# Optimization experiments

Measured on AMD Instinct MI355X. Metric: run time of the kernel, lower is better.

Reference implementation:

```python
import jax, jax.numpy as jnp
import numpy as np

B, N, E, K, H = 4, 2048, 512, 16, 8
EMB = 2 * E  # MultiheadAttention embed_dim = input_enc * 2


def setup_inputs() -> dict:
    key = jax.random.key(0)
    ks = jax.random.split(key, 6)
    s = 0.02
    return {
        "x": jax.random.normal(ks[0], (B, N, E), jnp.float32),
        "x_enc": jax.random.normal(ks[1], (B, N, EMB), jnp.float32),
        "w_in": jax.random.normal(ks[2], (3 * EMB, EMB), jnp.float32) * s,
        "b_in": jnp.zeros((3 * EMB,), jnp.float32),
        "w_out": jax.random.normal(ks[3], (EMB, EMB), jnp.float32) * s,
        "b_out": jnp.zeros((EMB,), jnp.float32),
        "k": K,
    }


def _knn_mean(x, k):
    # x: (B, N, E). torch code transposes to (B, E, N) and treats the E channel
    # rows as the 'points' for kNN (distance matrix is (B, E, E)).
    xt = jnp.swapaxes(x, 1, 2)                      # (B, E, N)
    sq = jnp.sum(xt * xt, axis=-1)                  # (B, E)
    dist = sq[:, :, None] + sq[:, None, :] - 2.0 * jnp.einsum("ben,bfn->bef", xt, xt)
    idx = jax.lax.top_k(-dist, k)[1]                # (B, E, k) smallest distances
    # fused gather + mean: avoid the (B, E, E, N) expand from the torch code
    nbrs = jnp.take_along_axis(xt[:, None, :, :], idx[:, :, :, None], axis=2)  # (B, E, k, N)
    return jnp.swapaxes(jnp.mean(nbrs, axis=2), 1, 2)  # (B, N, E)


def _mha(q, kv, w_in, b_in, w_out, b_out, h):
    # faithful torch nn.MultiheadAttention (batch_first) forward
    wq, wk, wv = jnp.split(w_in, 3, axis=0)
    bq, bk, bv = jnp.split(b_in, 3, axis=0)
    Q = q @ wq.T + bq
    Kt = kv @ wk.T + bk
    V = kv @ wv.T + bv
    b, l, emb = Q.shape
    m = Kt.shape[1]
    d = emb // h

    def split_heads(t):
        return t.reshape(t.shape[0], t.shape[1], h, d).transpose(0, 2, 1, 3)

    Qh, Kh, Vh = split_heads(Q), split_heads(Kt), split_heads(V)
    scores = jnp.einsum("bhld,bhmd->bhlm", Qh, Kh) / jnp.sqrt(jnp.float32(d))
    att = jax.nn.softmax(scores, axis=-1)
    o = jnp.einsum("bhlm,bhmd->bhld", att, Vh)      # (B, H, L, d)
    o = o.transpose(0, 2, 1, 3).reshape(b, l, emb)
    return o @ w_out.T + b_out


def reference(x, x_enc, w_in, b_in, w_out, b_out, k):
    b, n, e = x.shape
    x_knn = _knn_mean(x, k)                          # (B, N, E)
    cat = jnp.concatenate([jnp.swapaxes(x, 1, 2), jnp.swapaxes(x_knn, 1, 2)], axis=-1)  # (B, E, 2N)
    # faithful to torch .view(-1, 2*E, N): row-interleaving reshape, NOT a transpose
    q = jnp.swapaxes(cat.reshape(b, 2 * e, n), 1, 2)  # (B, N, 2E)
    attn = _mha(q, x_enc, w_in, b_in, w_out, b_out, H)  # (B, N, 2E)
    return jnp.concatenate([q, attn], axis=1)         # (B, 2N, 2E)
```

## Files before the change

### kernel.cpp

```cpp
#include <hip/hip_runtime.h>
#include <hip/hip_bf16.h>

#define B_ 4
#define N_ 2048
#define E_ 512
#define EMB_ 1024
#define H_ 8
#define D_ 128
#define KNN_ 16

typedef short short8_t __attribute__((ext_vector_type(8)));
typedef short short4_t __attribute__((ext_vector_type(4)));
typedef float float2_t __attribute__((ext_vector_type(2)));
typedef float float4_t __attribute__((ext_vector_type(4)));
typedef float float16_t __attribute__((ext_vector_type(16)));
typedef unsigned int uint2_t __attribute__((ext_vector_type(2)));
typedef unsigned int uint4_t __attribute__((ext_vector_type(4)));

__device__ __forceinline__ short f2bf(float f) {
  unsigned u = __float_as_uint(f);
  unsigned r = u + 0x7fffu + ((u >> 16) & 1u);
  return (short)(r >> 16);
}

__device__ __forceinline__ unsigned pk2bf(float a, float b) {
  float2 f; f.x = a; f.y = b;
  __hip_bfloat162 h = __float22bfloat162_rn(f);
  return *(unsigned*)&h;
}

__device__ __forceinline__ float fexp2(float x) {
  return __builtin_amdgcn_exp2f(x);
}

__device__ __forceinline__ void gload16(const short* g, short* l) {
  __builtin_amdgcn_global_load_lds(
      (const __attribute__((address_space(1))) void*)g,
      (__attribute__((address_space(3))) void*)l, 16, 0, 0);
}

__device__ __forceinline__ float tree16(const float* __restrict__ bs) {
  float t1[8], t2[4];
#pragma unroll
  for (int l = 0; l < 8; l++) t1[l] = __fadd_rn(bs[2 * l], bs[2 * l + 1]);
#pragma unroll
  for (int l = 0; l < 4; l++) t2[l] = __fadd_rn(t1[2 * l], t1[2 * l + 1]);
  return __fadd_rn(__fadd_rn(t2[0], t2[1]), __fadd_rn(t2[2], t2[3]));
}

__global__ __launch_bounds__(64) void k_gram_sqnp(const float* __restrict__ x,
                                                  float* __restrict__ g,
                                                  float* __restrict__ part) {
  const int bx = blockIdx.x;
  const int b = blockIdx.y;
  if (bx >= 272) {
    const int idx = (bx - 272) * 64 + threadIdx.x;
    const int e = idx & (E_ - 1), blk = idx >> 9;
    const float* p = x + (size_t)b * N_ * E_ + (size_t)blk * 128 * E_ + e;
    float lane[16];
#pragma unroll
    for (int l = 0; l < 16; l++) {
      float pr[8];
#pragma unroll
      for (int j = 0; j < 8; j++) {
        float v = p[(size_t)(j * 16 + l) * E_];
        pr[j] = __fmul_rn(v, v);
      }
      float s01 = __fadd_rn(pr[0], pr[1]);
      float s23 = __fadd_rn(pr[2], pr[3]);
      float s45 = __fadd_rn(pr[4], pr[5]);
      float s67 = __fadd_rn(pr[6], pr[7]);
      lane[l] = __fadd_rn(__fadd_rn(s01, s23), __fadd_rn(s45, s67));
    }
    float bb[8];
#pragma unroll
    for (int l = 0; l < 8; l++) bb[l] = __fadd_rn(lane[l], lane[l + 8]);
    float cc[4];
#pragma unroll
    for (int l = 0; l < 4; l++) cc[l] = __fadd_rn(bb[l], bb[l + 4]);
    part[((size_t)b * E_ + e) * 16 + blk] =
        __fadd_rn(__fadd_rn(cc[0], cc[1]), __fadd_rn(cc[2], cc[3]));
    return;
  }
  __shared__ __align__(16) float Xs[2][32][68];
  int p = bx >> 1;
  const int jh = bx & 1;
  int ti = 0;
  while (p >= 16 - ti) { p -= 16 - ti; ti++; }
  const int tj = ti + p;
  const int i0 = ti * 32, j0 = tj * 32 + jh * 16;
  const int lane = threadIdx.x;
  const int li = lane & 7, lj = lane >> 3;
  const int cq = lane & 7, rn = lane >> 3;
  const int qj = lane & 3, rj = lane >> 2;
  const float* xb = x + (size_t)b * N_ * E_;

  float acc[4][2];
#pragma unroll
  for (int u = 0; u < 4; u++) { acc[u][0] = 0.f; acc[u][1] = 0.f; }

  float4_t gi[4], gj[2];
#pragma unroll
  for (int ps = 0; ps < 4; ps++) {
    const int n = ps * 8 + rn;
    gi[ps] = *(const float4_t*)(xb + (size_t)n * E_ + i0 + cq * 4);
  }
#pragma unroll
  for (int s = 0; s < 2; s++) {
    const int n = s * 16 + rj;
    gj[s] = *(const float4_t*)(xb + (size_t)n * E_ + j0 + qj * 4);
  }
#pragma unroll
  for (int ps = 0; ps < 4; ps++) {
    const int nn = ps * 8 + rn;
    *(float4_t*)&Xs[0][nn][(cq * 4) ^ ((nn & 7) << 2)] = gi[ps];
  }
#pragma unroll
  for (int s = 0; s < 2; s++) {
    const int nn = s * 16 + rj;
    *(float4_t*)&Xs[0][nn][32 + ((qj * 4) ^ ((nn & 3) << 2))] = gj[s];
  }

  for (int c = 0; c < 64; c++) {
    const int buf = c & 1;
    if (c < 63) {
      const int nb = (c + 1) * 32;
#pragma unroll
      for (int ps = 0; ps < 4; ps++) {
        const int n = nb + ps * 8 + rn;
        gi[ps] = *(const float4_t*)(xb + (size_t)n * E_ + i0 + cq * 4);
      }
#pragma unroll
      for (int s = 0; s < 2; s++) {
        const int n = nb + s * 16 + rj;
        gj[s] = *(const float4_t*)(xb + (size_t)n * E_ + j0 + qj * 4);
      }
    }
#pragma unroll
    for (int nn = 0; nn < 32; nn++) {
      const float4_t va = *(const float4_t*)
          &Xs[buf][nn][(li * 4) ^ ((nn & 7) << 2)];
      const float2_t vb = *(const float2_t*)
          &Xs[buf][nn][32 + (((lj >> 1) * 4) ^ ((nn & 3) << 2)) + (lj & 1) * 2];
#pragma unroll
      for (int u = 0; u < 4; u++) {
        acc[u][0] = __fadd_rn(acc[u][0], __fmul_rn(va[u], vb[0]));
        acc[u][1] = __fadd_rn(acc[u][1], __fmul_rn(va[u], vb[1]));
      }
    }
    if (c < 63) {
#pragma unroll
      for (int ps = 0; ps < 4; ps++) {
        const int nn = ps * 8 + rn;
        *(float4_t*)&Xs[buf ^ 1][nn][(cq * 4) ^ ((nn & 7) << 2)] = gi[ps];
      }
#pragma unroll
      for (int s = 0; s < 2; s++) {
        const int nn = s * 16 + rj;
        *(float4_t*)&Xs[buf ^ 1][nn][32 + ((qj * 4) ^ ((nn & 3) << 2))] = gj[s];
      }
    }
  }
  float* gb = g + (size_t)b * E_ * E_;
#pragma unroll
  for (int u = 0; u < 4; u++) {
#pragma unroll
    for (int v = 0; v < 2; v++) {
      const int i = i0 + li * 4 + u, j = j0 + lj * 2 + v;
      gb[(size_t)i * E_ + j] = acc[u][v];
      if (ti != tj) gb[(size_t)j * E_ + i] = acc[u][v];
    }
  }
}

__global__ __launch_bounds__(64) void k_topk(const float* __restrict__ part,
                                             const float* __restrict__ g,
                                             int* __restrict__ idxout) {
  const int bi = blockIdx.x;
  const int b = bi >> 9, i = bi & (E_ - 1);
  const int lane = threadIdx.x;
  const float* gb = g + ((size_t)b * E_ + i) * E_;
  const float* pb = part + ((size_t)b << 9) * 16;
  const float sqi = tree16(pb + (size_t)i * 16);
  const int base = lane * 8;
  float v[8];
#pragma unroll
  for (int u = 0; u < 8; u++) {
    const float sqj = tree16(pb + (size_t)(base + u) * 16);
    v[u] = __fsub_rn(__fadd_rn(sqi, sqj), __fmul_rn(2.0f, gb[base + u]));
  }
  for (int t = 0; t < KNN_; t++) {
    float best = 3.0e38f; int bidx = E_;
#pragma unroll
    for (int u = 0; u < 8; u++) {
      if (v[u] < best) { best = v[u]; bidx = base + u; }
    }
#pragma unroll
    for (int off = 1; off < 64; off <<= 1) {
      float ov = __shfl_xor(best, off);
      int oi = __shfl_xor(bidx, off);
      if (ov < best || (ov == best && oi < bidx)) { best = ov; bidx = oi; }
    }
    if (lane == 0) idxout[(size_t)bi * KNN_ + t] = bidx;
#pragma unroll
    for (int u = 0; u < 8; u++) {
      if (bidx == base + u) v[u] = 3.0e38f;
    }
  }
}

__global__ __launch_bounds__(256) void k_knnmean(const float* __restrict__ x,
                                                 const int* __restrict__ idx,
                                                 float* __restrict__ out,
                                                 short* __restrict__ Xq) {
  const int n = blockIdx.x, b = blockIdx.y;
  const int tid = threadIdx.x;
  __shared__ float xrow[E_];
  const float* xr = x + ((size_t)b * N_ + n) * E_;
  for (int i = tid; i < E_; i += 256) xrow[i] = xr[i];
  __syncthreads();
  float* orow = out + ((size_t)b * (2 * N_) + n) * EMB_;
  unsigned* qrow = (unsigned*)(Xq + ((size_t)b * N_ + n) * EMB_);
  for (int i = tid; i < E_; i += 256) {
    const int* id = idx + ((size_t)b * E_ + i) * KNN_;
    float s = 0.f;
#pragma unroll
    for (int t = 0; t < KNN_; t++) s = __fadd_rn(s, xrow[id[t]]);
    float2 w; w.x = xrow[i]; w.y = s * (1.0f / 16.0f);
    *(float2*)&orow[2 * i] = w;
    qrow[i] = pk2bf(w.x, w.y);
  }
}

__global__ __launch_bounds__(256) void k_cvt3(const float* __restrict__ xe,
                                              const float* __restrict__ wi,
                                              const float* __restrict__ wo,
                                              short* __restrict__ Xe,
                                              short* __restrict__ Wi,
                                              short* __restrict__ Wo) {
  const size_t t = (size_t)blockIdx.x * 256 + threadIdx.x;
  const float* src; short* dst;
  if (t < 1048576u) { src = xe + t * 8; dst = Xe + t * 8; }
  else if (t < 1048576u + 393216u) {
    const size_t r = t - 1048576u; src = wi + r * 8; dst = Wi + r * 8;
  } else {
    const size_t r = t - 1441792u; src = wo + r * 8; dst = Wo + r * 8;
  }
  float4 a = *(const float4*)src, b = *(const float4*)(src + 4);
  short8_t v;
  v[0] = f2bf(a.x); v[1] = f2bf(a.y); v[2] = f2bf(a.z); v[3] = f2bf(a.w);
  v[4] = f2bf(b.x); v[5] = f2bf(b.y); v[6] = f2bf(b.z); v[7] = f2bf(b.w);
  *(short8_t*)dst = v;
}

__global__ __launch_bounds__(256) void k_gemm_qkv(
    const short* __restrict__ Xq, const short* __restrict__ Xe,
    const short* __restrict__ Win, const float* __restrict__ b_in,
    short* __restrict__ Qb, short* __restrict__ Kb, short* __restrict__ Vb) {
  __shared__ __align__(16) short As[128 * 64];
  __shared__ __align__(16) short Bs[128 * 64];
  const int tid = threadIdx.x;
  const int z = blockIdx.z;
  const short* X = (z == 0) ? Xq : Xe;
  const short* W = Win + (size_t)z * EMB_ * EMB_;
  const float* bias = b_in + z * EMB_;
  const int row0 = blockIdx.x * 128, col0 = blockIdx.y * 128;
  const int l = tid & 63, lg = l >> 4, lq = l & 15;
  const int w = tid >> 6, wm = w >> 1, wn = w & 1;
  float4_t acc[4][4];
#pragma unroll
  for (int i = 0; i < 4; i++)
#pragma unroll
    for (int j = 0; j < 4; j++) {
      acc[i][j][0] = 0.f; acc[i][j][1] = 0.f; acc[i][j][2] = 0.f; acc[i][j][3] = 0.f;
    }

  int soff[4], ldsb[4];
#pragma unroll
  for (int ii = 0; ii < 4; ii++) {
    const int cid = ii * 256 + tid;
    const int r = cid >> 3, c = cid & 7;
    soff[ii] = r * EMB_ + ((c * 8) ^ ((r & 7) << 3));
    ldsb[ii] = (ii * 256 + w * 64) * 8;
  }
  const short* Xb = X + (size_t)row0 * EMB_;
  const short* Wb = W + (size_t)col0 * EMB_;

  for (int kt = 0; kt < 16; kt++) {
    __syncthreads();
#pragma unroll
    for (int ii = 0; ii < 4; ii++) {
      gload16(Xb + soff[ii] + kt * 64, As + ldsb[ii]);
      gload16(Wb + soff[ii] + kt * 64, Bs + ldsb[ii]);
    }
    __syncthreads();
#pragma unroll
    for (int kk = 0; kk < 2; kk++) {
      short8_t af[4], bf[4];
#pragma unroll
      for (int mi = 0; mi < 4; mi++) {
        const int r = wm * 64 + mi * 16 + lq;
        af[mi] = *(const short8_t*)&As[r * 64 + ((kk * 32 + lg * 8) ^ ((r & 7) << 3))];
      }
#pragma unroll
      for (int ni = 0; ni < 4; ni++) {
        const int r = wn * 64 + ni * 16 + lq;
        bf[ni] = *(const short8_t*)&Bs[r * 64 + ((kk * 32 + lg * 8) ^ ((r & 7) << 3))];
      }
#pragma unroll
      for (int mi = 0; mi < 4; mi++)
#pragma unroll
        for (int ni = 0; ni < 4; ni++)
          acc[mi][ni] = __builtin_amdgcn_mfma_f32_16x16x32_bf16(af[mi], bf[ni], acc[mi][ni], 0, 0, 0);
    }
  }
  short* Yb = (z == 0) ? Qb : ((z == 1) ? Kb : Vb);
#pragma unroll
  for (int ni = 0; ni < 4; ni++) {
    const int col = col0 + wn * 64 + ni * 16 + lq;
    const float bv = bias[col];
#pragma unroll
    for (int mi = 0; mi < 4; mi++) {
#pragma unroll
      for (int j = 0; j < 4; j++) {
        const int m = row0 + wm * 64 + mi * 16 + lg * 4 + j;
        const float v = acc[mi][ni][j] + bv;
        if (z < 2) {
          Yb[(size_t)m * EMB_ + col] = f2bf(v);
        } else {
          const int b2 = m >> 11, n2 = m & (N_ - 1);
          Yb[((size_t)b2 * EMB_ + col) * N_ + n2] = f2bf(v);
        }
      }
    }
  }
}

__global__ __launch_bounds__(256) void k_gemm_out(
    const short* __restrict__ X, const short* __restrict__ W,
    const float* __restrict__ bias, float* __restrict__ Yf) {
  __shared__ __align__(16) short As[128 * 64];
  __shared__ __align__(16) short Bs[128 * 64];
  const int tid = threadIdx.x;
  const int row0 = blockIdx.x * 128, col0 = blockIdx.y * 128;
  const int l = tid & 63, lg = l >> 4, lq = l & 15;
  const int w = tid >> 6, wm = w >> 1, wn = w & 1;
  float4_t acc[4][4];
#pragma unroll
  for (int i = 0; i < 4; i++)
#pragma unroll
    for (int j = 0; j < 4; j++) {
      acc[i][j][0] = 0.f; acc[i][j][1] = 0.f; acc[i][j][2] = 0.f; acc[i][j][3] = 0.f;
    }

  int soff[4], ldsb[4];
#pragma unroll
  for (int ii = 0; ii < 4; ii++) {
    const int cid = ii * 256 + tid;
    const int r = cid >> 3, c = cid & 7;
    soff[ii] = r * EMB_ + ((c * 8) ^ ((r & 7) << 3));
    ldsb[ii] = (ii * 256 + w * 64) * 8;
  }
  const short* Xb = X + (size_t)row0 * EMB_;
  const short* Wb = W + (size_t)col0 * EMB_;

  for (int kt = 0; kt < 16; kt++) {
    __syncthreads();
#pragma unroll
    for (int ii = 0; ii < 4; ii++) {
      gload16(Xb + soff[ii] + kt * 64, As + ldsb[ii]);
      gload16(Wb + soff[ii] + kt * 64, Bs + ldsb[ii]);
    }
    __syncthreads();
#pragma unroll
    for (int kk = 0; kk < 2; kk++) {
      short8_t af[4], bf[4];
#pragma unroll
      for (int mi = 0; mi < 4; mi++) {
        const int r = wm * 64 + mi * 16 + lq;
        af[mi] = *(const short8_t*)&As[r * 64 + ((kk * 32 + lg * 8) ^ ((r & 7) << 3))];
      }
#pragma unroll
      for (int ni = 0; ni < 4; ni++) {
        const int r = wn * 64 + ni * 16 + lq;
        bf[ni] = *(const short8_t*)&Bs[r * 64 + ((kk * 32 + lg * 8) ^ ((r & 7) << 3))];
      }
#pragma unroll
      for (int mi = 0; mi < 4; mi++)
#pragma unroll
        for (int ni = 0; ni < 4; ni++)
          acc[mi][ni] = __builtin_amdgcn_mfma_f32_16x16x32_bf16(af[mi], bf[ni], acc[mi][ni], 0, 0, 0);
    }
  }
#pragma unroll
  for (int ni = 0; ni < 4; ni++) {
    const int col = col0 + wn * 64 + ni * 16 + lq;
    const float bv = bias[col];
#pragma unroll
    for (int mi = 0; mi < 4; mi++) {
#pragma unroll
      for (int j = 0; j < 4; j++) {
        const int m = row0 + wm * 64 + mi * 16 + lg * 4 + j;
        const int b2 = m >> 11, n2 = m & (N_ - 1);
        Yf[((size_t)b2 * 2 * N_ + N_ + n2) * EMB_ + col] = acc[mi][ni][j] + bv;
      }
    }
  }
}

__global__ __launch_bounds__(256, 2) void k_flash_bf16(
    const short* __restrict__ Qg, const short* __restrict__ Kg,
    const short* __restrict__ Vtg, short* __restrict__ Og) {
  __shared__ __align__(16) short Ks[2][64 * 128];
  __shared__ __align__(16) short Vs[2][128 * 64];
  const int tid = threadIdx.x;
  const int w = tid >> 6, l = tid & 63;
  const int hi = l >> 5, l5 = l & 31;
  const int bid = blockIdx.x;
  const int bh = (bid & 7) * 4 + ((bid >> 3) >> 4);
  const int rt = (bid >> 3) & 15;
  const int b = bh >> 3, h = bh & 7;
  const float c1 = 0.08838834764831845f * 1.4426950408889634f;
  const size_t bhoff = (size_t)b * N_ * EMB_ + (size_t)h * D_;
  const int ksw = (l5 & 15) << 3;
  const int psw = (l5 & 7) << 3;

  int ksrc[4], vsrc[4], ldb[4];
#pragma unroll
  for (int ii = 0; ii < 4; ii++) {
    const int cid = ii * 256 + tid;
    const int kr = cid >> 4, kc = cid & 15;
    const int vr = cid >> 3, vc = cid & 7;
    ksrc[ii] = kr * EMB_ + ((kc * 8) ^ ((kr & 15) << 3));
    vsrc[ii] = vr * N_ + ((vc * 8) ^ ((vr & 7) << 3));
    ldb[ii] = (ii * 256 + w * 64) * 8;
  }
  const short* Kt0 = Kg + bhoff;
  const short* Vt0 = Vtg + (size_t)b * EMB_ * N_ + (size_t)(h * D_) * N_;

  short8_t qf[8];
  {
    const short* qrow = Qg + bhoff + (size_t)(rt * 128 + w * 32 + l5) * EMB_;
#pragma unroll
    for (int s = 0; s < 8; s++)
      qf[s] = *(const short8_t*)(qrow + s * 16 + hi * 8);
  }
  float16_t oacc[4];
#pragma unroll
  for (int dg = 0; dg < 4; dg++)
#pragma unroll
    for (int r = 0; r < 16; r++) oacc[dg][r] = 0.f;
  float m = -3.0e38f, lsum = 0.f;

#pragma unroll
  for (int ii = 0; ii < 4; ii++) {
    gload16(Kt0 + ksrc[ii], &Ks[0][ldb[ii]]);
    gload16(Vt0 + vsrc[ii], &Vs[0][ldb[ii]]);
  }
  __syncthreads();

  for (int kt = 0; kt < N_ / 64; kt++) {
    const int buf = kt & 1;
    if (kt + 1 < N_ / 64) {
      const short* Kt = Kt0 + (size_t)((kt + 1) * 64) * EMB_;
      const short* Vt = Vt0 + (kt + 1) * 64;
#pragma unroll
      for (int ii = 0; ii < 4; ii++) {
        gload16(Kt + ksrc[ii], &Ks[buf ^ 1][ldb[ii]]);
        gload16(Vt + vsrc[ii], &Vs[buf ^ 1][ldb[ii]]);
      }
    }

    float16_t s0, s1;
#pragma unroll
    for (int r = 0; r < 16; r++) { s0[r] = 0.f; s1[r] = 0.f; }
    __builtin_amdgcn_s_setprio(1);
#pragma unroll
    for (int s = 0; s < 8; s++) {
      const int col = (s * 16 + hi * 8) ^ ksw;
      short8_t kf0 = *(const short8_t*)&Ks[buf][l5 * 128 + col];
      short8_t kf1 = *(const short8_t*)&Ks[buf][(32 + l5) * 128 + col];
      s0 = __builtin_amdgcn_mfma_f32_32x32x16_bf16(kf0, qf[s], s0, 0, 0, 0);
      s1 = __builtin_amdgcn_mfma_f32_32x32x16_bf16(kf1, qf[s], s1, 0, 0, 0);
    }
    __builtin_amdgcn_s_setprio(0);

    float tm = s0[0];
#pragma unroll
    for (int r = 1; r < 16; r++) tm = fmaxf(tm, s0[r]);
#pragma unroll
    for (int r = 0; r < 16; r++) tm = fmaxf(tm, s1[r]);
    tm = fmaxf(tm, __shfl_xor(tm, 32));
    if (__any(tm > m + 62.7f)) {
      const float mn = fmaxf(m, tm);
      const float alpha = fexp2((m - mn) * c1);
      m = mn;
      lsum *= alpha;
#pragma unroll
      for (int dg = 0; dg < 4; dg++)
#pragma unroll
        for (int r = 0; r < 16; r++) oacc[dg][r] *= alpha;
    }
    const float mc1 = m * c1;
    float ps = 0.f;
    unsigned w0[8], w1[8];
#pragma unroll
    for (int t = 0; t < 4; t++) {
      float p0 = fexp2(__builtin_fmaf(s0[4 * t + 0], c1, -mc1));
      float p1 = fexp2(__builtin_fmaf(s0[4 * t + 1], c1, -mc1));
      float p2 = fexp2(__builtin_fmaf(s0[4 * t + 2], c1, -mc1));
      float p3 = fexp2(__builtin_fmaf(s0[4 * t + 3], c1, -mc1));
      ps += (p0 + p1) + (p2 + p3);
      w0[t] = pk2bf(p0, p1); w1[t] = pk2bf(p2, p3);
    }
#pragma unroll
    for (int t = 0; t < 4; t++) {
      float p0 = fexp2(__builtin_fmaf(s1[4 * t + 0], c1, -mc1));
      float p1 = fexp2(__builtin_fmaf(s1[4 * t + 1], c1, -mc1));
      float p2 = fexp2(__builtin_fmaf(s1[4 * t + 2], c1, -mc1));
      float p3 = fexp2(__builtin_fmaf(s1[4 * t + 3], c1, -mc1));
      ps += (p0 + p1) + (p2 + p3);
      w0[4 + t] = pk2bf(p0, p1); w1[4 + t] = pk2bf(p2, p3);
    }
    ps += __shfl_xor(ps, 32);
    lsum += ps;

    short8_t pf[4];
#pragma unroll
    for (int ks = 0; ks < 4; ks++) {
      const int t0 = 2 * ks, t1 = 2 * ks + 1;
      uint2_t ra = __builtin_amdgcn_permlane32_swap(w0[t0], w0[t1], false, false);
      uint2_t rb = __builtin_amdgcn_permlane32_swap(w1[t0], w1[t1], false, false);
      uint4_t pw; pw[0] = ra[0]; pw[1] = rb[0]; pw[2] = ra[1]; pw[3] = rb[1];
      pf[ks] = *(short8_t*)&pw;
    }

    __builtin_amdgcn_s_setprio(1);
#pragma unroll
    for (int ks = 0; ks < 4; ks++) {
      const int col = (ks * 16 + hi * 8) ^ psw;
#pragma unroll
      for (int dg = 0; dg < 4; dg++) {
        short8_t vf = *(const short8_t*)&Vs[buf][(dg * 32 + l5) * 64 + col];
        oacc[dg] = __builtin_amdgcn_mfma_f32_32x32x16_bf16(vf, pf[ks], oacc[dg], 0, 0, 0);
      }
    }
    __builtin_amdgcn_s_setprio(0);

    __syncthreads();
  }

  const float linv = 1.0f / lsum;
  short* orow = Og + bhoff + (size_t)(rt * 128 + w * 32 + l5) * EMB_;
#pragma unroll
  for (int dg = 0; dg < 4; dg++) {
#pragma unroll
    for (int g = 0; g < 4; g++) {
      float p0 = oacc[dg][4 * g + 0] * linv;
      float p1 = oacc[dg][4 * g + 1] * linv;
      float p2 = oacc[dg][4 * g + 2] * linv;
      float p3 = oacc[dg][4 * g + 3] * linv;
      uint2 ow; ow.x = pk2bf(p0, p1); ow.y = pk2bf(p2, p3);
      *(uint2*)&orow[dg * 32 + g * 8 + hi * 4] = ow;
    }
  }
}

extern "C" void kernel_launch(void* const* d_in, const int* in_sizes, int n_in,
                              void* d_out, int out_size, void* d_ws, size_t ws_size,
                              hipStream_t stream) {
  const float* x     = (const float*)d_in[0];
  const float* x_enc = (const float*)d_in[1];
  const float* w_in  = (const float*)d_in[2];
  const float* b_in  = (const float*)d_in[3];
  const float* w_out = (const float*)d_in[4];
  const float* b_out = (const float*)d_in[5];
  float* out = (float*)d_out;
  char* wsb = (char*)d_ws;

  const size_t oG    = 0;
  const size_t oSq   = oG + (size_t)B_ * E_ * E_ * 4;
  const size_t oPart = oSq + (size_t)B_ * E_ * 4;
  const size_t oIdx  = oPart + (size_t)B_ * E_ * 16 * 4;
  const size_t oXq   = (oIdx + (size_t)B_ * E_ * KNN_ * 4 + 255) & ~(size_t)255;
  const size_t sB    = (size_t)B_ * N_ * EMB_ * 2;
  const size_t oXe   = oXq + sB;
  const size_t oWin  = oXe + sB;
  const size_t oWo   = oWin + 3ull * EMB_ * EMB_ * 2;
  const size_t oQ    = oWo + (size_t)EMB_ * EMB_ * 2;
  const size_t oK    = oQ + sB;
  const size_t oV    = oK + sB;
  const size_t oO    = oV + sB;
  const size_t need  = oO + sB;

  float* g    = (float*)(wsb + oG);
  float* part = (float*)(wsb + oPart);
  int*   idx  = (int*)(wsb + oIdx);
  short* Xq   = (short*)(wsb + oXq);
  short* Xe   = (short*)(wsb + oXe);
  short* Win  = (short*)(wsb + oWin);
  short* Wo   = (short*)(wsb + oWo);
  short* Qb   = (short*)(wsb + oQ);
  short* Kb   = (short*)(wsb + oK);
  short* Vb   = (short*)(wsb + oV);
  short* Ob   = (ws_size >= need) ? (short*)(wsb + oO) : Qb;

  k_gram_sqnp<<<dim3(400, B_), 64, 0, stream>>>(x, g, part);
  k_topk<<<dim3(B_ * E_), 64, 0, stream>>>(part, g, idx);
  k_knnmean<<<dim3(N_, B_), 256, 0, stream>>>(x, idx, out, Xq);

  k_cvt3<<<dim3(6144), 256, 0, stream>>>(x_enc, w_in, w_out, Xe, Win, Wo);

  k_gemm_qkv<<<dim3(64, 8, 3), 256, 0, stream>>>(Xq, Xe, Win, b_in, Qb, Kb, Vb);

  k_flash_bf16<<<dim3(512), 256, 0, stream>>>(Qb, Kb, Vb, Ob);

  k_gemm_out<<<dim3(64, 8), 256, 0, stream>>>(Ob, Wo, b_out, out);
}
```

Before: 320.4 us.

## Split attention over two key halves and merge partial softmax results

Flash attention now splits the 2048-key range into two halves, launching 1024 blocks instead of 512. Each block writes a bf16 partial output plus per-row max and sum, and a new combine kernel rescales and merges the two halves. The K/V double buffer is dropped so the smaller shared memory allows four blocks per CU, which raises occupancy and lets other waves hide load latency. In exchange it adds an extra kernel pass over the outputs, an extra bf16 rounding of the partial outputs, and the Xq/Xe/gram buffers are reused as scratch.

```diff
diff --git a/kernel.cpp b/kernel.cpp
--- a/kernel.cpp
+++ b/kernel.cpp
@@ -27,6 +27,10 @@
   float2 f; f.x = a; f.y = b;
   __hip_bfloat162 h = __float22bfloat162_rn(f);
   return *(unsigned*)&h;
+}
+
+__device__ __forceinline__ float bf2f(short s) {
+  return __uint_as_float(((unsigned)(unsigned short)s) << 16);
 }
 
 __device__ __forceinline__ float fexp2(float x) {
@@ -408,17 +412,20 @@
   }
 }
 
-__global__ __launch_bounds__(256, 2) void k_flash_bf16(
+__global__ __launch_bounds__(256, 4) void k_flash_split(
     const short* __restrict__ Qg, const short* __restrict__ Kg,
-    const short* __restrict__ Vtg, short* __restrict__ Og) {
-  __shared__ __align__(16) short Ks[2][64 * 128];
-  __shared__ __align__(16) short Vs[2][128 * 64];
+    const short* __restrict__ Vtg, short* __restrict__ O0,
+    short* __restrict__ O1, float2* __restrict__ ml) {
+  __shared__ __align__(16) short Ks[64 * 128];
+  __shared__ __align__(16) short Vs[128 * 64];
   const int tid = threadIdx.x;
   const int w = tid >> 6, l = tid & 63;
   const int hi = l >> 5, l5 = l & 31;
   const int bid = blockIdx.x;
-  const int bh = (bid & 7) * 4 + ((bid >> 3) >> 4);
-  const int rt = (bid >> 3) & 15;
+  const int r = bid >> 3;
+  const int half = r & 1;
+  const int rt = (r >> 1) & 15;
+  const int bh = (bid & 7) * 4 + (r >> 5);
   const int b = bh >> 3, h = bh & 7;
   const float c1 = 0.08838834764831845f * 1.4426950408889634f;
   const size_t bhoff = (size_t)b * N_ * EMB_ + (size_t)h * D_;
@@ -435,8 +442,9 @@
     vsrc[ii] = vr * N_ + ((vc * 8) ^ ((vr & 7) << 3));
     ldb[ii] = (ii * 256 + w * 64) * 8;
   }
-  const short* Kt0 = Kg + bhoff;
-  const short* Vt0 = Vtg + (size_t)b * EMB_ * N_ + (size_t)(h * D_) * N_;
+  const short* Kt0 = Kg + bhoff + (size_t)(half * 1024) * EMB_;
+  const short* Vt0 = Vtg + (size_t)b * EMB_ * N_ + (size_t)(h * D_) * N_
+                     + half * 1024;
 
   short8_t qf[8];
   {
@@ -449,37 +457,29 @@
 #pragma unroll
   for (int dg = 0; dg < 4; dg++)
 #pragma unroll
-    for (int r = 0; r < 16; r++) oacc[dg][r] = 0.f;
+    for (int rr = 0; rr < 16; rr++) oacc[dg][rr] = 0.f;
   float m = -3.0e38f, lsum = 0.f;
 
-#pragma unroll
-  for (int ii = 0; ii < 4; ii++) {
-    gload16(Kt0 + ksrc[ii], &Ks[0][ldb[ii]]);
-    gload16(Vt0 + vsrc[ii], &Vs[0][ldb[ii]]);
-  }
-  __syncthreads();
-
-  for (int kt = 0; kt < N_ / 64; kt++) {
-    const int buf = kt & 1;
-    if (kt + 1 < N_ / 64) {
-      const short* Kt = Kt0 + (size_t)((kt + 1) * 64) * EMB_;
-      const short* Vt = Vt0 + (kt + 1) * 64;
-#pragma unroll
-      for (int ii = 0; ii < 4; ii++) {
-        gload16(Kt + ksrc[ii], &Ks[buf ^ 1][ldb[ii]]);
-        gload16(Vt + vsrc[ii], &Vs[buf ^ 1][ldb[ii]]);
-      }
-    }
+  for (int t = 0; t < 16; t++) {
+    __syncthreads();
+    const short* Kt = Kt0 + (size_t)(t * 64) * EMB_;
+    const short* Vt = Vt0 + t * 64;
+#pragma unroll
+    for (int ii = 0; ii < 4; ii++) {
+      gload16(Kt + ksrc[ii], Ks + ldb[ii]);
+      gload16(Vt + vsrc[ii], Vs + ldb[ii]);
+    }
+    __syncthreads();
 
     float16_t s0, s1;
 #pragma unroll
-    for (int r = 0; r < 16; r++) { s0[r] = 0.f; s1[r] = 0.f; }
+    for (int rr = 0; rr < 16; rr++) { s0[rr] = 0.f; s1[rr] = 0.f; }
     __builtin_amdgcn_s_setprio(1);
 #pragma unroll
     for (int s = 0; s < 8; s++) {
       const int col = (s * 16 + hi * 8) ^ ksw;
-      short8_t kf0 = *(const short8_t*)&Ks[buf][l5 * 128 + col];
-      short8_t kf1 = *(const short8_t*)&Ks[buf][(32 + l5) * 128 + col];
+      short8_t kf0 = *(const short8_t*)&Ks[l5 * 128 + col];
+      short8_t kf1 = *(const short8_t*)&Ks[(32 + l5) * 128 + col];
       s0 = __builtin_amdgcn_mfma_f32_32x32x16_bf16(kf0, qf[s], s0, 0, 0, 0);
       s1 = __builtin_amdgcn_mfma_f32_32x32x16_bf16(kf1, qf[s], s1, 0, 0, 0);
     }
@@ -487,9 +487,9 @@
 
     float tm = s0[0];
 #pragma unroll
-    for (int r = 1; r < 16; r++) tm = fmaxf(tm, s0[r]);
-#pragma unroll
-    for (int r = 0; r < 16; r++) tm = fmaxf(tm, s1[r]);
+    for (int rr = 1; rr < 16; rr++) tm = fmaxf(tm, s0[rr]);
+#pragma unroll
+    for (int rr = 0; rr < 16; rr++) tm = fmaxf(tm, s1[rr]);
     tm = fmaxf(tm, __shfl_xor(tm, 32));
     if (__any(tm > m + 62.7f)) {
       const float mn = fmaxf(m, tm);
@@ -499,28 +499,28 @@
 #pragma unroll
       for (int dg = 0; dg < 4; dg++)
 #pragma unroll
-        for (int r = 0; r < 16; r++) oacc[dg][r] *= alpha;
+        for (int rr = 0; rr < 16; rr++) oacc[dg][rr] *= alpha;
     }
     const float mc1 = m * c1;
     float ps = 0.f;
     unsigned w0[8], w1[8];
 #pragma unroll
-    for (int t = 0; t < 4; t++) {
-      float p0 = fexp2(__builtin_fmaf(s0[4 * t + 0], c1, -mc1));
-      float p1 = fexp2(__builtin_fmaf(s0[4 * t + 1], c1, -mc1));
-      float p2 = fexp2(__builtin_fmaf(s0[4 * t + 2], c1, -mc1));
-      float p3 = fexp2(__builtin_fmaf(s0[4 * t + 3], c1, -mc1));
+    for (int t2 = 0; t2 < 4; t2++) {
+      float p0 = fexp2(__builtin_fmaf(s0[4 * t2 + 0], c1, -mc1));
+      float p1 = fexp2(__builtin_fmaf(s0[4 * t2 + 1], c1, -mc1));
+      float p2 = fexp2(__builtin_fmaf(s0[4 * t2 + 2], c1, -mc1));
+      float p3 = fexp2(__builtin_fmaf(s0[4 * t2 + 3], c1, -mc1));
       ps += (p0 + p1) + (p2 + p3);
-      w0[t] = pk2bf(p0, p1); w1[t] = pk2bf(p2, p3);
-    }
-#pragma unroll
-    for (int t = 0; t < 4; t++) {
-      float p0 = fexp2(__builtin_fmaf(s1[4 * t + 0], c1, -mc1));
-      float p1 = fexp2(__builtin_fmaf(s1[4 * t + 1], c1, -mc1));
-      float p2 = fexp2(__builtin_fmaf(s1[4 * t + 2], c1, -mc1));
-      float p3 = fexp2(__builtin_fmaf(s1[4 * t + 3], c1, -mc1));
+      w0[t2] = pk2bf(p0, p1); w1[t2] = pk2bf(p2, p3);
+    }
+#pragma unroll
+    for (int t2 = 0; t2 < 4; t2++) {
+      float p0 = fexp2(__builtin_fmaf(s1[4 * t2 + 0], c1, -mc1));
+      float p1 = fexp2(__builtin_fmaf(s1[4 * t2 + 1], c1, -mc1));
+      float p2 = fexp2(__builtin_fmaf(s1[4 * t2 + 2], c1, -mc1));
+      float p3 = fexp2(__builtin_fmaf(s1[4 * t2 + 3], c1, -mc1));
       ps += (p0 + p1) + (p2 + p3);
-      w0[4 + t] = pk2bf(p0, p1); w1[4 + t] = pk2bf(p2, p3);
+      w0[4 + t2] = pk2bf(p0, p1); w1[4 + t2] = pk2bf(p2, p3);
     }
     ps += __shfl_xor(ps, 32);
     lsum += ps;
@@ -541,17 +541,16 @@
       const int col = (ks * 16 + hi * 8) ^ psw;
 #pragma unroll
       for (int dg = 0; dg < 4; dg++) {
-        short8_t vf = *(const short8_t*)&Vs[buf][(dg * 32 + l5) * 64 + col];
+        short8_t vf = *(const short8_t*)&Vs[(dg * 32 + l5) * 64 + col];
         oacc[dg] = __builtin_amdgcn_mfma_f32_32x32x16_bf16(vf, pf[ks], oacc[dg], 0, 0, 0);
       }
     }
     __builtin_amdgcn_s_setprio(0);
-
-    __syncthreads();
   }
 
   const float linv = 1.0f / lsum;
-  short* orow = Og + bhoff + (size_t)(rt * 128 + w * 32 + l5) * EMB_;
+  const int row = rt * 128 + w * 32 + l5;
+  short* orow = (half ? O1 : O0) + bhoff + (size_t)row * EMB_;
 #pragma unroll
   for (int dg = 0; dg < 4; dg++) {
 #pragma unroll
@@ -564,6 +563,36 @@
       *(uint2*)&orow[dg * 32 + g * 8 + hi * 4] = ow;
     }
   }
+  if (hi == 0) {
+    float2 v; v.x = m; v.y = lsum;
+    ml[(size_t)half * B_ * H_ * N_ + ((size_t)b * H_ + h) * N_ + row] = v;
+  }
+}
+
+__global__ __launch_bounds__(256) void k_comb(const float2* __restrict__ ml,
+                                              short* __restrict__ O0,
+                                              const short* __restrict__ O1) {
+  const int n = blockIdx.x, b = blockIdx.y;
+  const int t = threadIdx.x;
+  const int e0 = t * 4, h = e0 >> 7;
+  const float c1 = 0.08838834764831845f * 1.4426950408889634f;
+  const size_t mlh = ((size_t)b * H_ + h) * N_ + n;
+  const float2 v0 = ml[mlh];
+  const float2 v1 = ml[(size_t)B_ * H_ * N_ + mlh];
+  const float M = fmaxf(v0.x, v1.x);
+  float w0 = v0.y * fexp2((v0.x - M) * c1);
+  float w1 = v1.y * fexp2((v1.x - M) * c1);
+  const float inv = 1.f / (w0 + w1);
+  w0 *= inv; w1 *= inv;
+  const size_t off = ((size_t)b * N_ + n) * EMB_ + e0;
+  short4_t a = *(short4_t*)(O0 + off);
+  short4_t c = *(const short4_t*)(O1 + off);
+  float o0 = bf2f(a[0]) * w0 + bf2f(c[0]) * w1;
+  float o1 = bf2f(a[1]) * w0 + bf2f(c[1]) * w1;
+  float o2 = bf2f(a[2]) * w0 + bf2f(c[2]) * w1;
+  float o3 = bf2f(a[3]) * w0 + bf2f(c[3]) * w1;
+  uint2 ow; ow.x = pk2bf(o0, o1); ow.y = pk2bf(o2, o3);
+  *(uint2*)(O0 + off) = ow;
 }
 
 extern "C" void kernel_launch(void* const* d_in, const int* in_sizes, int n_in,
@@ -590,8 +619,6 @@
   const size_t oQ    = oWo + (size_t)EMB_ * EMB_ * 2;
   const size_t oK    = oQ + sB;
   const size_t oV    = oK + sB;
-  const size_t oO    = oV + sB;
-  const size_t need  = oO + sB;
 
   float* g    = (float*)(wsb + oG);
   float* part = (float*)(wsb + oPart);
@@ -603,7 +630,7 @@
   short* Qb   = (short*)(wsb + oQ);
   short* Kb   = (short*)(wsb + oK);
   short* Vb   = (short*)(wsb + oV);
-  short* Ob   = (ws_size >= need) ? (short*)(wsb + oO) : Qb;
+  float2* ml  = (float2*)(wsb + oG);
 
   k_gram_sqnp<<<dim3(400, B_), 64, 0, stream>>>(x, g, part);
   k_topk<<<dim3(B_ * E_), 64, 0, stream>>>(part, g, idx);
@@ -613,7 +640,8 @@
 
   k_gemm_qkv<<<dim3(64, 8, 3), 256, 0, stream>>>(Xq, Xe, Win, b_in, Qb, Kb, Vb);
 
-  k_flash_bf16<<<dim3(512), 256, 0, stream>>>(Qb, Kb, Vb, Ob);
-
-  k_gemm_out<<<dim3(64, 8), 256, 0, stream>>>(Ob, Wo, b_out, out);
-}
+  k_flash_split<<<dim3(1024), 256, 0, stream>>>(Qb, Kb, Vb, Xq, Xe, ml);
+  k_comb<<<dim3(N_, B_), 256, 0, stream>>>(ml, Xq, Xe);
+
+  k_gemm_out<<<dim3(64, 8), 256, 0, stream>>>(Xq, Wo, b_out, out);
+}
```

New measurement: 612.6 us. 1.91x slower.
